# Optimization experiments

Measured on AMD Instinct MI355X. Metric: run time of the kernel, lower is better.

Reference implementation:

```python
import jax, jax.numpy as jnp
import numpy as np

N = 100000   # nodes
E = 1600000  # edges (before self-loops)
F = 128      # num_features
H = 128      # hidden_dim
EPS = 1e-5   # BatchNorm eps


def setup_inputs() -> dict:
    key = jax.random.key(0)
    ks = jax.random.split(key, 8)
    x = jax.random.normal(ks[0], (N, F), dtype=jnp.float32)
    edge_index = jax.random.randint(ks[1], (2, E), 0, N, dtype=jnp.int64)

    def lin(k, din, dout):
        s = 1.0 / np.sqrt(din)
        kw, kb = jax.random.split(k)
        W = jax.random.uniform(kw, (din, dout), jnp.float32, -s, s)
        b = jax.random.uniform(kb, (dout,), jnp.float32, -s, s)
        return W, b

    W1, b1 = lin(ks[2], F, H)
    W2, b2 = lin(ks[3], H, H)
    W3, b3 = lin(ks[4], H, H)
    Wc, bc = lin(ks[5], H, 2)

    def bn_params():
        return (jnp.ones((H,), jnp.float32), jnp.zeros((H,), jnp.float32),
                jnp.zeros((H,), jnp.float32), jnp.ones((H,), jnp.float32))

    g1, be1, rm1, rv1 = bn_params()
    g2, be2, rm2, rv2 = bn_params()
    g3, be3, rm3, rv3 = bn_params()

    return {"x": x, "edge_index": edge_index,
            "W1": W1, "b1": b1, "W2": W2, "b2": b2, "W3": W3, "b3": b3,
            "g1": g1, "be1": be1, "rm1": rm1, "rv1": rv1,
            "g2": g2, "be2": be2, "rm2": rm2, "rv2": rv2,
            "g3": g3, "be3": be3, "rm3": rm3, "rv3": rv3,
            "Wc": Wc, "bc": bc}


def _gcn_norm(edge_index, num_nodes):
    # add self-loops, compute symmetric normalization (PyG GCNConv default)
    loop = jnp.arange(num_nodes, dtype=edge_index.dtype)
    src = jnp.concatenate([edge_index[0], loop])
    dst = jnp.concatenate([edge_index[1], loop])
    deg = jax.ops.segment_sum(jnp.ones_like(dst, dtype=jnp.float32), dst,
                              num_segments=num_nodes)
    dinv = jnp.where(deg > 0, jax.lax.rsqrt(deg), 0.0)
    norm = dinv[src] * dinv[dst]  # [E+N]
    return src, dst, norm


def _gcn_conv(x, W, b, src, dst, norm, num_nodes):
    h = x @ W                              # [N, H] linear first
    msg = h[src] * norm[:, None]           # gather + scale  [E+N, H]
    out = jax.ops.segment_sum(msg, dst, num_segments=num_nodes)  # scatter-add
    return out + b


def _bn_eval(x, g, be, rm, rv):
    return (x - rm) * jax.lax.rsqrt(rv + EPS) * g + be


def reference(x, edge_index,
              W1, b1, W2, b2, W3, b3,
              g1, be1, rm1, rv1,
              g2, be2, rm2, rv2,
              g3, be3, rm3, rv3,
              Wc, bc):
    n = x.shape[0]
    src, dst, norm = _gcn_norm(edge_index, n)
    h = _gcn_conv(x, W1, b1, src, dst, norm, n)
    h = _bn_eval(jax.nn.relu(h), g1, be1, rm1, rv1)
    # dropout: identity in eval mode
    h = _gcn_conv(h, W2, b2, src, dst, norm, n)
    h = _bn_eval(jax.nn.relu(h), g2, be2, rm2, rv2)
    h = _gcn_conv(h, W3, b3, src, dst, norm, n)
    h = _bn_eval(jax.nn.relu(h), g3, be3, rm3, rv3)
    return h @ Wc + bc  # [N, 2]
```

## Files before the change

kernel.cpp:

```cpp
#include <hip/hip_runtime.h>
#include <hip/hip_fp16.h>

#define BN_EPS 1e-5f
#define CHUNK 4096
#define BBITS 7

typedef _Float16 half8 __attribute__((ext_vector_type(8)));
typedef float f32x4 __attribute__((ext_vector_type(4)));

__device__ __forceinline__ float4 f4zero() { return make_float4(0.f, 0.f, 0.f, 0.f); }


__global__ __launch_bounds__(256) void k_pack_hist(const float* __restrict__ W1,
                                                   const float* __restrict__ W2,
                                                   const float* __restrict__ W3,
                                                   _Float16* __restrict__ pW,
                                                   const int* __restrict__ dst,
                                                   int* __restrict__ tableT,
                                                   int* __restrict__ counts,
                                                   int nA, int nbuck, int e) {
    __shared__ int h[1024];
    int tid = threadIdx.x;
    if (blockIdx.x < 24) {
        int t = blockIdx.x * 256 + tid;
        int wi = t >> 11;
        int tt = t & 2047;
        const float* W = (wi == 0) ? W1 : ((wi == 1) ? W2 : W3);
        int kc = tt >> 9;
        int rem = tt & 511;
        int ct = rem >> 6;
        int lane = rem & 63;
        int q = lane >> 4;
        int col = ct * 16 + (lane & 15);
        half8 hh;
#pragma unroll
        for (int j = 0; j < 8; ++j)
            hh[j] = (_Float16)W[(kc * 32 + q * 8 + j) * 128 + col];
        *(half8*)(pW + (size_t)t * 8) = hh;
        return;
    }
    int blk = blockIdx.x - 24;
    for (int k = tid; k < 1024; k += 256) h[k] = 0;
    __syncthreads();
    int base = blk * CHUNK;
    if (base + CHUNK <= e && (e & 3) == 0) {
        const int4* d4 = (const int4*)(dst + base);
#pragma unroll
        for (int t = 0; t < CHUNK / 1024; ++t) {
            int4 d = d4[t * 256 + tid];
            atomicAdd(&h[d.x >> BBITS], 1);
            atomicAdd(&h[d.y >> BBITS], 1);
            atomicAdd(&h[d.z >> BBITS], 1);
            atomicAdd(&h[d.w >> BBITS], 1);
            atomicAdd(&counts[d.x], 1);
            atomicAdd(&counts[d.y], 1);
            atomicAdd(&counts[d.z], 1);
            atomicAdd(&counts[d.w], 1);
        }
    } else {
        for (int i = base + tid; i < e && i < base + CHUNK; i += 256) {
            int d = dst[i];
            atomicAdd(&h[d >> BBITS], 1);
            atomicAdd(&counts[d], 1);
        }
    }
    __syncthreads();
    for (int k = tid; k < nbuck; k += 256)
        tableT[(size_t)k * nA + blk] = h[k];
}


__global__ __launch_bounds__(1024) void k_scan_block(const int* __restrict__ in,
                                                     int* __restrict__ outp,
                                                     int* __restrict__ partials, int len) {
    __shared__ int s[1024];
    int t = threadIdx.x;
    int gid = blockIdx.x * 1024 + t;
    int v = (gid < len) ? in[gid] : 0;
    int x = v;
    s[t] = x;
    __syncthreads();
    for (int d = 1; d < 1024; d <<= 1) {
        int y = (t >= d) ? s[t - d] : 0;
        __syncthreads();
        x += y;
        s[t] = x;
        __syncthreads();
    }
    if (gid < len) outp[gid] = x - v;
    if (t == 1023) partials[blockIdx.x] = x;
}

__global__ __launch_bounds__(256) void k_scan_addp_dinv(int* __restrict__ data,
                                                        const int* __restrict__ partials,
                                                        int len,
                                                        const int* __restrict__ counts,
                                                        float* __restrict__ dinv,
                                                        int n, int gT) {
    __shared__ int red[256];
    int tid = threadIdx.x;
    if ((int)blockIdx.x >= gT) {
        int node = ((int)blockIdx.x - gT) * 256 + tid;
        if (node < n) dinv[node] = rsqrtf((float)(counts[node] + 1));
        return;
    }
    int K = blockIdx.x >> 2;
    int s = 0;
    for (int t = tid; t < K; t += 256) s += partials[t];
    red[tid] = s;
    __syncthreads();
    for (int d = 128; d > 0; d >>= 1) {
        if (tid < d) red[tid] += red[tid + d];
        __syncthreads();
    }
    int gid = blockIdx.x * 256 + tid;
    if (gid < len) data[gid] += red[0];
}


template <bool AF32>
__device__ __forceinline__ void gemm_body(int bid, int tid, char* smem,
                                          const void* __restrict__ Av,
                                          const _Float16* __restrict__ pW,
                                          const float* __restrict__ dinv,
                                          uint4* __restrict__ C, int n) {
    uint4* sW = (uint4*)smem;
    {
        const uint4* gW = (const uint4*)pW;
#pragma unroll
        for (int i = 0; i < 8; ++i) sW[tid + 256 * i] = gW[tid + 256 * i];
    }
    __syncthreads();

    int wave = tid >> 6, lane = tid & 63;
    int quad = lane >> 4, l16 = lane & 15;
    int row0 = bid * 64 + wave * 16;
    int arow = row0 + l16;
    int arowc = (arow < n) ? arow : (n - 1);

    half8 af[4];
    if (AF32) {
        const float* A = (const float*)Av + (size_t)arowc * 128 + quad * 8;
#pragma unroll
        for (int kc = 0; kc < 4; ++kc) {
            float4 lo = *(const float4*)(A + kc * 32);
            float4 hi = *(const float4*)(A + kc * 32 + 4);
            half8 h;
            h[0] = (_Float16)lo.x; h[1] = (_Float16)lo.y;
            h[2] = (_Float16)lo.z; h[3] = (_Float16)lo.w;
            h[4] = (_Float16)hi.x; h[5] = (_Float16)hi.y;
            h[6] = (_Float16)hi.z; h[7] = (_Float16)hi.w;
            af[kc] = h;
        }
    } else {
        const _Float16* A = (const _Float16*)Av + (size_t)arowc * 128 + quad * 8;
#pragma unroll
        for (int kc = 0; kc < 4; ++kc)
            af[kc] = *(const half8*)(A + kc * 32);
    }

    f32x4 acc[8];
#pragma unroll
    for (int ct = 0; ct < 8; ++ct) acc[ct] = (f32x4){0.f, 0.f, 0.f, 0.f};

#pragma unroll
    for (int kc = 0; kc < 4; ++kc) {
#pragma unroll
        for (int ct = 0; ct < 8; ++ct) {
            half8 bf = *(half8*)&sW[(kc * 8 + ct) * 64 + lane];
            acc[ct] = __builtin_amdgcn_mfma_f32_16x16x32_f16(af[kc], bf, acc[ct], 0, 0, 0);
        }
    }

    __syncthreads();

    _Float16* eb = (_Float16*)smem + wave * 16 * 136;
    float dv[4];
#pragma unroll
    for (int r = 0; r < 4; ++r) {
        int rr = row0 + quad * 4 + r;
        dv[r] = dinv[(rr < n) ? rr : (n - 1)];
    }
#pragma unroll
    for (int ct = 0; ct < 8; ++ct)
#pragma unroll
        for (int r = 0; r < 4; ++r)
            eb[(quad * 4 + r) * 136 + ct * 16 + l16] = (_Float16)(acc[ct][r] * dv[r]);

#pragma unroll
    for (int i = 0; i < 4; ++i) {
        int linear = i * 64 + lane;
        int r = linear >> 4, c = linear & 15;
        uint4 v = *(uint4*)((char*)eb + r * 272 + c * 16);
        int row = row0 + r;
        if (row < n) C[(size_t)row * 16 + c] = v;
    }
}

__global__ __launch_bounds__(256) void k_gemm_mfma(const void* __restrict__ Av,
                                                   const _Float16* __restrict__ pW,
                                                   const float* __restrict__ dinv,
                                                   uint4* __restrict__ C, int n) {
    __shared__ char smem[32768];
    gemm_body<false>(blockIdx.x, threadIdx.x, smem, Av, pW, dinv, C, n);
}


__global__ __launch_bounds__(256) void k_scatter_gemm(const int* __restrict__ src,
                                                      const int* __restrict__ dst,
                                                      const int* __restrict__ tableT,
                                                      int2* __restrict__ bed,
                                                      int nA, int nbuck, int e,
                                                      const float* __restrict__ x,
                                                      const _Float16* __restrict__ pW,
                                                      const float* __restrict__ dinv,
                                                      uint4* __restrict__ C, int n) {
    __shared__ char smem[32768];
    int tid = threadIdx.x;
    if ((int)blockIdx.x >= nA) {
        gemm_body<true>((int)blockIdx.x - nA, tid, smem, x, pW, dinv, C, n);
        return;
    }
    int* cur = (int*)smem;
    int blk = blockIdx.x;
    for (int k = tid; k < nbuck; k += 256)
        cur[k] = tableT[(size_t)k * nA + blk];
    __syncthreads();
    int base = blk * CHUNK;
    if (base + CHUNK <= e && (e & 3) == 0) {
        const int4* s4 = (const int4*)(src + base);
        const int4* d4 = (const int4*)(dst + base);
#pragma unroll
        for (int t = 0; t < CHUNK / 1024; ++t) {
            int4 s = s4[t * 256 + tid];
            int4 d = d4[t * 256 + tid];
            int p0 = atomicAdd(&cur[d.x >> BBITS], 1); bed[p0] = make_int2(s.x, d.x);
            int p1 = atomicAdd(&cur[d.y >> BBITS], 1); bed[p1] = make_int2(s.y, d.y);
            int p2 = atomicAdd(&cur[d.z >> BBITS], 1); bed[p2] = make_int2(s.z, d.z);
            int p3 = atomicAdd(&cur[d.w >> BBITS], 1); bed[p3] = make_int2(s.w, d.w);
        }
    } else {
        for (int i = base + tid; i < e && i < base + CHUNK; i += 256) {
            int d = dst[i];
            int p = atomicAdd(&cur[d >> BBITS], 1);
            bed[p] = make_int2(src[i], d);
        }
    }
}


__global__ __launch_bounds__(256) void k_rank_finalize(const int2* __restrict__ bed,
                                                       const int* __restrict__ tableT,
                                                       int2* __restrict__ offs2,
                                                       int* __restrict__ er,
                                                       unsigned int* __restrict__ bufAzero,
                                                       int nA, int nbuck, int n, int e) {
    __shared__ int lcnt[128];
    __shared__ int lscan[128];
    __shared__ int loff[128];
    int b = blockIdx.x, tid = threadIdx.x;
    if (tid < 128) lcnt[tid] = 0;
    __syncthreads();
    int start = tableT[(size_t)b * nA];
    int end = (b + 1 < nbuck) ? tableT[(size_t)(b + 1) * nA] : e;
    for (int i = start + tid; i < end; i += 256)
        atomicAdd(&lcnt[bed[i].y & 127], 1);
    __syncthreads();
    int padded = 0;
    if (tid < 128) {
        padded = (lcnt[tid] + 7) & ~7;
        lscan[tid] = padded;
    }
    __syncthreads();
    for (int d = 1; d < 128; d <<= 1) {
        int y = (tid < 128 && tid >= d) ? lscan[tid - d] : 0;
        __syncthreads();
        if (tid < 128) lscan[tid] += y;
        __syncthreads();
    }
    int ebase = start + (b << 10);
    if (tid < 128) {
        loff[tid] = lscan[tid] - padded;
        int node = (b << BBITS) + tid;
        if (node < n) {
            int c = lcnt[tid];
            int o = ebase + loff[tid];
            offs2[node] = make_int2(o, o + padded);
            for (int j = c; j < padded; ++j) er[o + j] = n << 8;
        }
    }
    if (b == 0 && tid < 64) bufAzero[tid] = 0u;
    __syncthreads();
    if (tid < 128) lcnt[tid] = 0;
    __syncthreads();
    for (int i = start + tid; i < end; i += 256) {
        int2 q = bed[i];
        int l = q.y & 127;
        int r = atomicAdd(&lcnt[l], 1);
        er[ebase + loff[l] + r] = q.x << 8;
    }
}


__device__ __forceinline__ void acc_row4(float4& aL, float4& aH, uint4 q) {
    asm("v_fma_mix_f32 %0, %1, 1.0, %0 op_sel:[0,0,0] op_sel_hi:[1,0,0]" : "+v"(aL.x) : "v"(q.x));
    asm("v_fma_mix_f32 %0, %1, 1.0, %0 op_sel:[1,0,0] op_sel_hi:[1,0,0]" : "+v"(aL.y) : "v"(q.x));
    asm("v_fma_mix_f32 %0, %1, 1.0, %0 op_sel:[0,0,0] op_sel_hi:[1,0,0]" : "+v"(aL.z) : "v"(q.y));
    asm("v_fma_mix_f32 %0, %1, 1.0, %0 op_sel:[1,0,0] op_sel_hi:[1,0,0]" : "+v"(aL.w) : "v"(q.y));
    asm("v_fma_mix_f32 %0, %1, 1.0, %0 op_sel:[0,0,0] op_sel_hi:[1,0,0]" : "+v"(aH.x) : "v"(q.z));
    asm("v_fma_mix_f32 %0, %1, 1.0, %0 op_sel:[1,0,0] op_sel_hi:[1,0,0]" : "+v"(aH.y) : "v"(q.z));
    asm("v_fma_mix_f32 %0, %1, 1.0, %0 op_sel:[0,0,0] op_sel_hi:[1,0,0]" : "+v"(aH.z) : "v"(q.w));
    asm("v_fma_mix_f32 %0, %1, 1.0, %0 op_sel:[1,0,0] op_sel_hi:[1,0,0]" : "+v"(aH.w) : "v"(q.w));
}


template <bool FUSE_CLS>
__global__ __launch_bounds__(256) void k_aggregate(const uint4* __restrict__ Ah,
                                                   const int2* __restrict__ offs2,
                                                   const int* __restrict__ er,
                                                   const float* __restrict__ dinv,
                                                   const float* __restrict__ bias,
                                                   const float* __restrict__ g,
                                                   const float* __restrict__ be,
                                                   const float* __restrict__ rm,
                                                   const float* __restrict__ rv,
                                                   uint4* __restrict__ Hout,
                                                   const float* __restrict__ Wc,
                                                   const float* __restrict__ bc,
                                                   float* __restrict__ out, int n) {
    int lane = threadIdx.x & 15;
    int node = blockIdx.x * 16 + (threadIdx.x >> 4);
    if (node >= n) return;

    const char* AhB = (const char*)Ah;
    unsigned int l16 = (unsigned int)lane * 16u;

    float4 aL = f4zero(), aH = f4zero();
    acc_row4(aL, aH, *(const uint4*)(AhB + (((unsigned int)node << 8) + l16)));

    int2 offc = offs2[node];
    int e0 = offc.x, e1 = offc.y;
    for (int e = e0; e < e1; e += 8) {
        int4 ra = *(const int4*)(er + e);
        int4 rb = *(const int4*)(er + e + 4);
        uint4 v0 = *(const uint4*)(AhB + ((unsigned int)ra.x + l16));
        uint4 v1 = *(const uint4*)(AhB + ((unsigned int)ra.y + l16));
        uint4 v2 = *(const uint4*)(AhB + ((unsigned int)ra.z + l16));
        uint4 v3 = *(const uint4*)(AhB + ((unsigned int)ra.w + l16));
        uint4 v4 = *(const uint4*)(AhB + ((unsigned int)rb.x + l16));
        uint4 v5 = *(const uint4*)(AhB + ((unsigned int)rb.y + l16));
        uint4 v6 = *(const uint4*)(AhB + ((unsigned int)rb.z + l16));
        uint4 v7 = *(const uint4*)(AhB + ((unsigned int)rb.w + l16));
        acc_row4(aL, aH, v0); acc_row4(aL, aH, v1); acc_row4(aL, aH, v2); acc_row4(aL, aH, v3);
        acc_row4(aL, aH, v4); acc_row4(aL, aH, v5); acc_row4(aL, aH, v6); acc_row4(aL, aH, v7);
    }

    float di = dinv[node];
    aL.x *= di; aL.y *= di; aL.z *= di; aL.w *= di;
    aH.x *= di; aH.y *= di; aH.z *= di; aH.w *= di;

    float4 bL  = ((const float4*)bias)[2 * lane], bH  = ((const float4*)bias)[2 * lane + 1];
    float4 gL  = ((const float4*)g)[2 * lane],    gH  = ((const float4*)g)[2 * lane + 1];
    float4 beL = ((const float4*)be)[2 * lane],   beH = ((const float4*)be)[2 * lane + 1];
    float4 rmL = ((const float4*)rm)[2 * lane],   rmH = ((const float4*)rm)[2 * lane + 1];
    float4 rvL = ((const float4*)rv)[2 * lane],   rvH = ((const float4*)rv)[2 * lane + 1];

    float4 oL, oH;
    float v;
    v = fmaxf(aL.x + bL.x, 0.f); oL.x = (v - rmL.x) * rsqrtf(rvL.x + BN_EPS) * gL.x + beL.x;
    v = fmaxf(aL.y + bL.y, 0.f); oL.y = (v - rmL.y) * rsqrtf(rvL.y + BN_EPS) * gL.y + beL.y;
    v = fmaxf(aL.z + bL.z, 0.f); oL.z = (v - rmL.z) * rsqrtf(rvL.z + BN_EPS) * gL.z + beL.z;
    v = fmaxf(aL.w + bL.w, 0.f); oL.w = (v - rmL.w) * rsqrtf(rvL.w + BN_EPS) * gL.w + beL.w;
    v = fmaxf(aH.x + bH.x, 0.f); oH.x = (v - rmH.x) * rsqrtf(rvH.x + BN_EPS) * gH.x + beH.x;
    v = fmaxf(aH.y + bH.y, 0.f); oH.y = (v - rmH.y) * rsqrtf(rvH.y + BN_EPS) * gH.y + beH.y;
    v = fmaxf(aH.z + bH.z, 0.f); oH.z = (v - rmH.z) * rsqrtf(rvH.z + BN_EPS) * gH.z + beH.z;
    v = fmaxf(aH.w + bH.w, 0.f); oH.w = (v - rmH.w) * rsqrtf(rvH.w + BN_EPS) * gH.w + beH.w;

    if (!FUSE_CLS) {
        __half2 p0 = __floats2half2_rn(oL.x, oL.y);
        __half2 p1 = __floats2half2_rn(oL.z, oL.w);
        __half2 p2 = __floats2half2_rn(oH.x, oH.y);
        __half2 p3 = __floats2half2_rn(oH.z, oH.w);
        uint4 u;
        u.x = *(unsigned int*)&p0;
        u.y = *(unsigned int*)&p1;
        u.z = *(unsigned int*)&p2;
        u.w = *(unsigned int*)&p3;
        Hout[(size_t)node * 16 + lane] = u;
    } else {
        const float4* Wv = (const float4*)Wc;
        float4 w0 = Wv[4 * lane];
        float4 w1 = Wv[4 * lane + 1];
        float4 w2 = Wv[4 * lane + 2];
        float4 w3 = Wv[4 * lane + 3];
        float p0 = oL.x * w0.x + oL.y * w0.z + oL.z * w1.x + oL.w * w1.z
                 + oH.x * w2.x + oH.y * w2.z + oH.z * w3.x + oH.w * w3.z;
        float p1 = oL.x * w0.y + oL.y * w0.w + oL.z * w1.y + oL.w * w1.w
                 + oH.x * w2.y + oH.y * w2.w + oH.z * w3.y + oH.w * w3.w;
#pragma unroll
        for (int d = 8; d >= 1; d >>= 1) {
            p0 += __shfl_down(p0, d, 16);
            p1 += __shfl_down(p1, d, 16);
        }
        if (lane == 0) {
            out[node * 2 + 0] = p0 + bc[0];
            out[node * 2 + 1] = p1 + bc[1];
        }
    }
}


extern "C" void kernel_launch(void* const* d_in, const int* in_sizes, int n_in,
                              void* d_out, int out_size, void* d_ws, size_t ws_size,
                              hipStream_t stream) {
    const float* x   = (const float*)d_in[0];
    const int*   ei  = (const int*)d_in[1];
    const float* W1  = (const float*)d_in[2];
    const float* b1  = (const float*)d_in[3];
    const float* W2  = (const float*)d_in[4];
    const float* b2  = (const float*)d_in[5];
    const float* W3  = (const float*)d_in[6];
    const float* b3  = (const float*)d_in[7];
    const float* g1  = (const float*)d_in[8];
    const float* be1 = (const float*)d_in[9];
    const float* rm1 = (const float*)d_in[10];
    const float* rv1 = (const float*)d_in[11];
    const float* g2  = (const float*)d_in[12];
    const float* be2 = (const float*)d_in[13];
    const float* rm2 = (const float*)d_in[14];
    const float* rv2 = (const float*)d_in[15];
    const float* g3  = (const float*)d_in[16];
    const float* be3 = (const float*)d_in[17];
    const float* rm3 = (const float*)d_in[18];
    const float* rv3 = (const float*)d_in[19];
    const float* Wc  = (const float*)d_in[20];
    const float* bc  = (const float*)d_in[21];
    float* out = (float*)d_out;

    int n = in_sizes[0] / 128;
    int e = in_sizes[1] / 2;
    const int* src = ei;
    const int* dst = ei + e;

    char* ws = (char*)d_ws;
    size_t off = 0;
    auto alloc = [&](size_t bytes) -> char* {
        char* p = ws + off;
        off += (bytes + 255) & ~(size_t)255;
        return p;
    };
    int nA    = (e + CHUNK - 1) / CHUNK;
    int nbuck = (n + (1 << BBITS) - 1) >> BBITS;
    int tlen  = nbuck * nA;
    int erCap = e + (nbuck << 10) + 64;

    char*      bufA     = (char*) alloc((size_t)(n + 1) * 256);
    char*      bufH     = (char*) alloc((size_t)n * 256);
    float*     dinv     = (float*)alloc((size_t)n * 4);
    int*       counts   = (int*)  alloc((size_t)n * 4);
    int2*      offs2    = (int2*) alloc((size_t)n * 8);
    int*       tableT   = (int*)  alloc((size_t)(tlen + 1) * 4);
    int*       parts    = (int*)  alloc(8192);
    int*       er       = (int*)  alloc((size_t)erCap * 4);
    _Float16*  pW       = (_Float16*)alloc(3 * 16384 * 2);
    (void)ws_size; (void)n_in; (void)out_size;

    int2* bed = (int2*)bufH;

    int nbT   = (tlen + 1023) / 1024;
    int gT    = (tlen + 255) / 256;
    int gD    = (n + 255) / 256;
    int gGemm = (n + 63) / 64;
    int gAgg  = (n + 15) / 16;

    hipMemsetAsync(counts, 0, (size_t)n * 4, stream);
    k_pack_hist<<<24 + nA, 256, 0, stream>>>(W1, W2, W3, pW, dst, tableT, counts,
                                             nA, nbuck, e);
    k_scan_block<<<nbT, 1024, 0, stream>>>(tableT, tableT, parts, tlen);
    k_scan_addp_dinv<<<gT + gD, 256, 0, stream>>>(tableT, parts, tlen, counts, dinv, n, gT);
    k_scatter_gemm<<<nA + gGemm, 256, 0, stream>>>(src, dst, tableT, bed, nA, nbuck, e,
                                                   x, pW, dinv, (uint4*)bufA, n);
    k_rank_finalize<<<nbuck, 256, 0, stream>>>(bed, tableT, offs2, er,
                                               (unsigned int*)(bufA + (size_t)n * 256),
                                               nA, nbuck, n, e);

    k_aggregate<false><<<gAgg, 256, 0, stream>>>((const uint4*)bufA, offs2, er, dinv,
                                                 b1, g1, be1, rm1, rv1, (uint4*)bufH,
                                                 nullptr, nullptr, nullptr, n);
    k_gemm_mfma<<<gGemm, 256, 0, stream>>>(bufH, pW + 16384, dinv, (uint4*)bufA, n);
    k_aggregate<false><<<gAgg, 256, 0, stream>>>((const uint4*)bufA, offs2, er, dinv,
                                                 b2, g2, be2, rm2, rv2, (uint4*)bufH,
                                                 nullptr, nullptr, nullptr, n);
    k_gemm_mfma<<<gGemm, 256, 0, stream>>>(bufH, pW + 32768, dinv, (uint4*)bufA, n);
    k_aggregate<true><<<gAgg, 256, 0, stream>>>((const uint4*)bufA, offs2, er, dinv,
                                                b3, g3, be3, rm3, rv3, nullptr,
                                                Wc, bc, out, n);
}
```

Baseline: 437.6 us.

## Compute degree normalization in rank-finalize and scale sources during aggregation

Drops the per-edge global atomic degree counting and the counts memset. Degrees are instead taken from the per-node bucket counts already computed in rank_finalize, which now writes dinv. Because dinv is no longer ready when the first GEMM runs, the source-side dinv scaling moves out of the GEMM epilogue into the aggregation loop. That loop now does an extra per-edge dinv gather and uses fma_mix with a scale. This trades 1.6M global atomics for 3×1.7M small gathers, and the padding entries index dinv[n], which is set to zero.

```diff
diff --git a/kernel.cpp b/kernel.cpp
--- a/kernel.cpp
+++ b/kernel.cpp
@@ -17,7 +17,6 @@
                                                    _Float16* __restrict__ pW,
                                                    const int* __restrict__ dst,
                                                    int* __restrict__ tableT,
-                                                   int* __restrict__ counts,
                                                    int nA, int nbuck, int e) {
     __shared__ int h[1024];
     int tid = threadIdx.x;
@@ -52,17 +51,10 @@
             atomicAdd(&h[d.y >> BBITS], 1);
             atomicAdd(&h[d.z >> BBITS], 1);
             atomicAdd(&h[d.w >> BBITS], 1);
-            atomicAdd(&counts[d.x], 1);
-            atomicAdd(&counts[d.y], 1);
-            atomicAdd(&counts[d.z], 1);
-            atomicAdd(&counts[d.w], 1);
         }
     } else {
-        for (int i = base + tid; i < e && i < base + CHUNK; i += 256) {
-            int d = dst[i];
-            atomicAdd(&h[d >> BBITS], 1);
-            atomicAdd(&counts[d], 1);
-        }
+        for (int i = base + tid; i < e && i < base + CHUNK; i += 256)
+            atomicAdd(&h[dst[i] >> BBITS], 1);
     }
     __syncthreads();
     for (int k = tid; k < nbuck; k += 256)
@@ -91,19 +83,10 @@
     if (t == 1023) partials[blockIdx.x] = x;
 }
 
-__global__ __launch_bounds__(256) void k_scan_addp_dinv(int* __restrict__ data,
-                                                        const int* __restrict__ partials,
-                                                        int len,
-                                                        const int* __restrict__ counts,
-                                                        float* __restrict__ dinv,
-                                                        int n, int gT) {
+__global__ __launch_bounds__(256) void k_scan_addp(int* __restrict__ data,
+                                                   const int* __restrict__ partials, int len) {
     __shared__ int red[256];
     int tid = threadIdx.x;
-    if ((int)blockIdx.x >= gT) {
-        int node = ((int)blockIdx.x - gT) * 256 + tid;
-        if (node < n) dinv[node] = rsqrtf((float)(counts[node] + 1));
-        return;
-    }
     int K = blockIdx.x >> 2;
     int s = 0;
     for (int t = tid; t < K; t += 256) s += partials[t];
@@ -122,7 +105,6 @@
 __device__ __forceinline__ void gemm_body(int bid, int tid, char* smem,
                                           const void* __restrict__ Av,
                                           const _Float16* __restrict__ pW,
-                                          const float* __restrict__ dinv,
                                           uint4* __restrict__ C, int n) {
     uint4* sW = (uint4*)smem;
     {
@@ -175,17 +157,11 @@
     __syncthreads();
 
     _Float16* eb = (_Float16*)smem + wave * 16 * 136;
-    float dv[4];
-#pragma unroll
-    for (int r = 0; r < 4; ++r) {
-        int rr = row0 + quad * 4 + r;
-        dv[r] = dinv[(rr < n) ? rr : (n - 1)];
-    }
 #pragma unroll
     for (int ct = 0; ct < 8; ++ct)
 #pragma unroll
         for (int r = 0; r < 4; ++r)
-            eb[(quad * 4 + r) * 136 + ct * 16 + l16] = (_Float16)(acc[ct][r] * dv[r]);
+            eb[(quad * 4 + r) * 136 + ct * 16 + l16] = (_Float16)(acc[ct][r]);
 
 #pragma unroll
     for (int i = 0; i < 4; ++i) {
@@ -199,10 +175,9 @@
 
 __global__ __launch_bounds__(256) void k_gemm_mfma(const void* __restrict__ Av,
                                                    const _Float16* __restrict__ pW,
-                                                   const float* __restrict__ dinv,
                                                    uint4* __restrict__ C, int n) {
     __shared__ char smem[32768];
-    gemm_body<false>(blockIdx.x, threadIdx.x, smem, Av, pW, dinv, C, n);
+    gemm_body<false>(blockIdx.x, threadIdx.x, smem, Av, pW, C, n);
 }
 
 
@@ -213,12 +188,11 @@
                                                       int nA, int nbuck, int e,
                                                       const float* __restrict__ x,
                                                       const _Float16* __restrict__ pW,
-                                                      const float* __restrict__ dinv,
                                                       uint4* __restrict__ C, int n) {
     __shared__ char smem[32768];
     int tid = threadIdx.x;
     if ((int)blockIdx.x >= nA) {
-        gemm_body<true>((int)blockIdx.x - nA, tid, smem, x, pW, dinv, C, n);
+        gemm_body<true>((int)blockIdx.x - nA, tid, smem, x, pW, C, n);
         return;
     }
     int* cur = (int*)smem;
@@ -253,6 +227,7 @@
                                                        const int* __restrict__ tableT,
                                                        int2* __restrict__ offs2,
                                                        int* __restrict__ er,
+                                                       float* __restrict__ dinv,
                                                        unsigned int* __restrict__ bufAzero,
                                                        int nA, int nbuck, int n, int e) {
     __shared__ int lcnt[128];
@@ -286,10 +261,12 @@
             int c = lcnt[tid];
             int o = ebase + loff[tid];
             offs2[node] = make_int2(o, o + padded);
+            dinv[node] = rsqrtf((float)(c + 1));
             for (int j = c; j < padded; ++j) er[o + j] = n << 8;
         }
     }
     if (b == 0 && tid < 64) bufAzero[tid] = 0u;
+    if (b == 0 && tid == 0) dinv[n] = 0.f;
     __syncthreads();
     if (tid < 128) lcnt[tid] = 0;
     __syncthreads();
@@ -313,8 +290,19 @@
     asm("v_fma_mix_f32 %0, %1, 1.0, %0 op_sel:[1,0,0] op_sel_hi:[1,0,0]" : "+v"(aH.w) : "v"(q.w));
 }
 
-
-template <bool FUSE_CLS>
+__device__ __forceinline__ void acc_row4s(float4& aL, float4& aH, uint4 q, float s) {
+    asm("v_fma_mix_f32 %0, %1, %2, %0 op_sel:[0,0,0] op_sel_hi:[1,0,0]" : "+v"(aL.x) : "v"(q.x), "v"(s));
+    asm("v_fma_mix_f32 %0, %1, %2, %0 op_sel:[1,0,0] op_sel_hi:[1,0,0]" : "+v"(aL.y) : "v"(q.x), "v"(s));
+    asm("v_fma_mix_f32 %0, %1, %2, %0 op_sel:[0,0,0] op_sel_hi:[1,0,0]" : "+v"(aL.z) : "v"(q.y), "v"(s));
+    asm("v_fma_mix_f32 %0, %1, %2, %0 op_sel:[1,0,0] op_sel_hi:[1,0,0]" : "+v"(aL.w) : "v"(q.y), "v"(s));
+    asm("v_fma_mix_f32 %0, %1, %2, %0 op_sel:[0,0,0] op_sel_hi:[1,0,0]" : "+v"(aH.x) : "v"(q.z), "v"(s));
+    asm("v_fma_mix_f32 %0, %1, %2, %0 op_sel:[1,0,0] op_sel_hi:[1,0,0]" : "+v"(aH.y) : "v"(q.z), "v"(s));
+    asm("v_fma_mix_f32 %0, %1, %2, %0 op_sel:[0,0,0] op_sel_hi:[1,0,0]" : "+v"(aH.z) : "v"(q.w), "v"(s));
+    asm("v_fma_mix_f32 %0, %1, %2, %0 op_sel:[1,0,0] op_sel_hi:[1,0,0]" : "+v"(aH.w) : "v"(q.w), "v"(s));
+}
+
+
+template <bool FUSE_CLS, bool SRC_SCALE>
 __global__ __launch_bounds__(256) void k_aggregate(const uint4* __restrict__ Ah,
                                                    const int2* __restrict__ offs2,
                                                    const int* __restrict__ er,
@@ -335,8 +323,13 @@
     const char* AhB = (const char*)Ah;
     unsigned int l16 = (unsigned int)lane * 16u;
 
+    float di = dinv[node];
     float4 aL = f4zero(), aH = f4zero();
-    acc_row4(aL, aH, *(const uint4*)(AhB + (((unsigned int)node << 8) + l16)));
+    {
+        uint4 qs = *(const uint4*)(AhB + (((unsigned int)node << 8) + l16));
+        if (SRC_SCALE) acc_row4s(aL, aH, qs, di);
+        else           acc_row4(aL, aH, qs);
+    }
 
     int2 offc = offs2[node];
     int e0 = offc.x, e1 = offc.y;
@@ -351,11 +344,25 @@
         uint4 v5 = *(const uint4*)(AhB + ((unsigned int)rb.y + l16));
         uint4 v6 = *(const uint4*)(AhB + ((unsigned int)rb.z + l16));
         uint4 v7 = *(const uint4*)(AhB + ((unsigned int)rb.w + l16));
-        acc_row4(aL, aH, v0); acc_row4(aL, aH, v1); acc_row4(aL, aH, v2); acc_row4(aL, aH, v3);
-        acc_row4(aL, aH, v4); acc_row4(aL, aH, v5); acc_row4(aL, aH, v6); acc_row4(aL, aH, v7);
-    }
-
-    float di = dinv[node];
+        if (SRC_SCALE) {
+            float d0 = dinv[(unsigned int)ra.x >> 8];
+            float d1 = dinv[(unsigned int)ra.y >> 8];
+            float d2 = dinv[(unsigned int)ra.z >> 8];
+            float d3 = dinv[(unsigned int)ra.w >> 8];
+            float d4 = dinv[(unsigned int)rb.x >> 8];
+            float d5 = dinv[(unsigned int)rb.y >> 8];
+            float d6 = dinv[(unsigned int)rb.z >> 8];
+            float d7 = dinv[(unsigned int)rb.w >> 8];
+            acc_row4s(aL, aH, v0, d0); acc_row4s(aL, aH, v1, d1);
+            acc_row4s(aL, aH, v2, d2); acc_row4s(aL, aH, v3, d3);
+            acc_row4s(aL, aH, v4, d4); acc_row4s(aL, aH, v5, d5);
+            acc_row4s(aL, aH, v6, d6); acc_row4s(aL, aH, v7, d7);
+        } else {
+            acc_row4(aL, aH, v0); acc_row4(aL, aH, v1); acc_row4(aL, aH, v2); acc_row4(aL, aH, v3);
+            acc_row4(aL, aH, v4); acc_row4(aL, aH, v5); acc_row4(aL, aH, v6); acc_row4(aL, aH, v7);
+        }
+    }
+
     aL.x *= di; aL.y *= di; aL.z *= di; aL.w *= di;
     aH.x *= di; aH.y *= di; aH.z *= di; aH.w *= di;
 
@@ -456,8 +463,7 @@
 
     char*      bufA     = (char*) alloc((size_t)(n + 1) * 256);
     char*      bufH     = (char*) alloc((size_t)n * 256);
-    float*     dinv     = (float*)alloc((size_t)n * 4);
-    int*       counts   = (int*)  alloc((size_t)n * 4);
+    float*     dinv     = (float*)alloc((size_t)(n + 1) * 4);
     int2*      offs2    = (int2*) alloc((size_t)n * 8);
     int*       tableT   = (int*)  alloc((size_t)(tlen + 1) * 4);
     int*       parts    = (int*)  alloc(8192);
@@ -469,30 +475,27 @@
 
     int nbT   = (tlen + 1023) / 1024;
     int gT    = (tlen + 255) / 256;
-    int gD    = (n + 255) / 256;
     int gGemm = (n + 63) / 64;
     int gAgg  = (n + 15) / 16;
 
-    hipMemsetAsync(counts, 0, (size_t)n * 4, stream);
-    k_pack_hist<<<24 + nA, 256, 0, stream>>>(W1, W2, W3, pW, dst, tableT, counts,
-                                             nA, nbuck, e);
+    k_pack_hist<<<24 + nA, 256, 0, stream>>>(W1, W2, W3, pW, dst, tableT, nA, nbuck, e);
     k_scan_block<<<nbT, 1024, 0, stream>>>(tableT, tableT, parts, tlen);
-    k_scan_addp_dinv<<<gT + gD, 256, 0, stream>>>(tableT, parts, tlen, counts, dinv, n, gT);
+    k_scan_addp<<<gT, 256, 0, stream>>>(tableT, parts, tlen);
     k_scatter_gemm<<<nA + gGemm, 256, 0, stream>>>(src, dst, tableT, bed, nA, nbuck, e,
-                                                   x, pW, dinv, (uint4*)bufA, n);
-    k_rank_finalize<<<nbuck, 256, 0, stream>>>(bed, tableT, offs2, er,
+                                                   x, pW, (uint4*)bufA, n);
+    k_rank_finalize<<<nbuck, 256, 0, stream>>>(bed, tableT, offs2, er, dinv,
                                                (unsigned int*)(bufA + (size_t)n * 256),
                                                nA, nbuck, n, e);
 
-    k_aggregate<false><<<gAgg, 256, 0, stream>>>((const uint4*)bufA, offs2, er, dinv,
-                                                 b1, g1, be1, rm1, rv1, (uint4*)bufH,
-                                                 nullptr, nullptr, nullptr, n);
-    k_gemm_mfma<<<gGemm, 256, 0, stream>>>(bufH, pW + 16384, dinv, (uint4*)bufA, n);
-    k_aggregate<false><<<gAgg, 256, 0, stream>>>((const uint4*)bufA, offs2, er, dinv,
-                                                 b2, g2, be2, rm2, rv2, (uint4*)bufH,
-                                                 nullptr, nullptr, nullptr, n);
-    k_gemm_mfma<<<gGemm, 256, 0, stream>>>(bufH, pW + 32768, dinv, (uint4*)bufA, n);
-    k_aggregate<true><<<gAgg, 256, 0, stream>>>((const uint4*)bufA, offs2, er, dinv,
-                                                b3, g3, be3, rm3, rv3, nullptr,
-                                                Wc, bc, out, n);
-}
+    k_aggregate<false, true><<<gAgg, 256, 0, stream>>>((const uint4*)bufA, offs2, er, dinv,
+                                                       b1, g1, be1, rm1, rv1, (uint4*)bufH,
+                                                       nullptr, nullptr, nullptr, n);
+    k_gemm_mfma<<<gGemm, 256, 0, stream>>>(bufH, pW + 16384, (uint4*)bufA, n);
+    k_aggregate<false, true><<<gAgg, 256, 0, stream>>>((const uint4*)bufA, offs2, er, dinv,
+                                                       b2, g2, be2, rm2, rv2, (uint4*)bufH,
+                                                       nullptr, nullptr, nullptr, n);
+    k_gemm_mfma<<<gGemm, 256, 0, stream>>>(bufH, pW + 32768, (uint4*)bufA, n);
+    k_aggregate<true, true><<<gAgg, 256, 0, stream>>>((const uint4*)bufA, offs2, er, dinv,
+                                                      b3, g3, be3, rm3, rv3, nullptr,
+                                                      Wc, bc, out, n);
+}
```

Measured after the change: 390.3 us. -10.8%, faster.
